# Kernel tuning notes

Hardware: AMD Instinct MI355X
Metric: run time of the kernel (lower is better)

Reference implementation:

```python
import jax, jax.numpy as jnp
import numpy as np

L, B, D = 2048, 8, 1024
EPS = 1e-5


def setup_inputs() -> dict:
    key = jax.random.key(0)
    k1, k2 = jax.random.split(key)
    x = jax.random.normal(k1, (L, B, D), dtype=jnp.float32)
    c = jnp.zeros((B, D), dtype=jnp.float32)
    # w_ufr: Linear(D, 3D); weight init normal(std=0.001), bias zero except
    # the reset-gate third which is filled with 2.0 (per the torch init).
    W = jax.random.normal(k2, (3 * D, D), dtype=jnp.float32) * 0.001
    b = jnp.zeros((3 * D,), dtype=jnp.float32).at[2 * D:].set(2.0)
    gamma = jnp.ones((D,), dtype=jnp.float32)
    beta = jnp.zeros((D,), dtype=jnp.float32)
    return {"x": x, "c": c, "W": W, "b": b, "gamma": gamma, "beta": beta}


def _layernorm(x, gamma, beta):
    mu = jnp.mean(x, axis=-1, keepdims=True)
    var = jnp.var(x, axis=-1, keepdims=True)
    return (x - mu) * jax.lax.rsqrt(var + EPS) * gamma + beta


def reference(x, c, W, b, gamma, beta):
    residual = x
    x_norm = _layernorm(x, gamma, beta)            # [L,B,D]
    ufr = jnp.einsum('lbd,ed->lbe', x_norm, W) + b  # [L,B,3D]
    u, f, r = jnp.split(ufr, 3, axis=-1)
    f_gate = jax.nn.sigmoid(f)
    r_gate = jax.nn.sigmoid(r)

    def step(c_prev, fu):
        f_t, u_t = fu
        c_t = f_t * c_prev + (1.0 - f_t) * u_t
        return c_t, c_t

    last_c, c_stack = jax.lax.scan(step, c, (f_gate, u))  # c_stack: [L,B,D]
    hs = r_gate * jnp.tanh(c_stack) + (1.0 - r_gate) * x_norm
    # dropout is identity in eval mode
    return residual + hs, last_c
```

## Files before the change

### kernel.cpp

```cpp
#include <hip/hip_runtime.h>
#include <hip/hip_bf16.h>

#define L_DIM 2048
#define B_DIM 8
#define D_DIM 1024
#define M_DIM (L_DIM * B_DIM)
#define N_DIM (3 * D_DIM)
#define K_DIM D_DIM
#define BD (B_DIM * D_DIM)
#define NCHUNK 64
#define CLEN (L_DIM / NCHUNK)

typedef __attribute__((ext_vector_type(8))) __bf16 bf16x8;
typedef __attribute__((ext_vector_type(4))) __bf16 bf16x4;
typedef __attribute__((ext_vector_type(4))) float f32x4;

#define GLOAD_LDS16(g, l)                                        \
  __builtin_amdgcn_global_load_lds(                              \
      (const __attribute__((address_space(1))) void*)(g),        \
      (__attribute__((address_space(3))) void*)(l), 16, 0, 0)

__device__ __forceinline__ float sigmoidf_(float v) {
  return 1.0f / (1.0f + __expf(-v));
}

__global__ __launch_bounds__(256) void ln_kernel(
    const float* __restrict__ x, const float* __restrict__ gamma,
    const float* __restrict__ beta, __bf16* __restrict__ xn) {
  const int row = blockIdx.x;
  const int tid = threadIdx.x;
  const float4 v = ((const float4*)(x + (size_t)row * D_DIM))[tid];
  float s  = v.x + v.y + v.z + v.w;
  float ss = v.x * v.x + v.y * v.y + v.z * v.z + v.w * v.w;
  #pragma unroll
  for (int off = 32; off > 0; off >>= 1) {
    s  += __shfl_xor(s, off);
    ss += __shfl_xor(ss, off);
  }
  __shared__ float sb[8];
  const int wid = tid >> 6, lane = tid & 63;
  if (lane == 0) { sb[wid] = s; sb[4 + wid] = ss; }
  __syncthreads();
  const float tot  = sb[0] + sb[1] + sb[2] + sb[3];
  const float tot2 = sb[4] + sb[5] + sb[6] + sb[7];
  const float mu  = tot * (1.0f / D_DIM);
  const float var = tot2 * (1.0f / D_DIM) - mu * mu;
  const float rstd = rsqrtf(var + 1e-5f);
  const float4 g  = ((const float4*)gamma)[tid];
  const float4 bt = ((const float4*)beta)[tid];
  bf16x4 o;
  o[0] = (__bf16)((v.x - mu) * rstd * g.x + bt.x);
  o[1] = (__bf16)((v.y - mu) * rstd * g.y + bt.y);
  o[2] = (__bf16)((v.z - mu) * rstd * g.z + bt.z);
  o[3] = (__bf16)((v.w - mu) * rstd * g.w + bt.w);
  ((bf16x4*)(xn + (size_t)row * D_DIM))[tid] = o;
}

__global__ __launch_bounds__(256) void wconv_kernel(
    const float* __restrict__ W, __bf16* __restrict__ Wb) {
  const size_t i = ((size_t)blockIdx.x * 256 + threadIdx.x) * 4;
  const float4 v = *(const float4*)(W + i);
  bf16x4 o;
  o[0] = (__bf16)v.x; o[1] = (__bf16)v.y; o[2] = (__bf16)v.z; o[3] = (__bf16)v.w;
  *(bf16x4*)(Wb + i) = o;
}

#define VMCNT(n) asm volatile("s_waitcnt vmcnt(" #n ")" ::: "memory")

__global__ __launch_bounds__(512, 4) void gemm256_kernel(
    const __bf16* __restrict__ A,
    const __bf16* __restrict__ Bm,
    const float* __restrict__ bias,
    __bf16* __restrict__ U, __bf16* __restrict__ FG, __bf16* __restrict__ RG) {
  __shared__ __bf16 lds[36864];
  const int tid = threadIdx.x;
  const int lane = tid & 63;
  const int wid = tid >> 6;
  const int wq = wid >> 1;
  const int wc = wid & 1;

  const int bid0 = blockIdx.x;
  const int bid = (bid0 & 7) * 192 + (bid0 >> 3);
  const int bm = bid / 24, bn = bid % 24;

#define BUFO(p) ((p) * 12288)

  const int srow  = tid >> 2;
  const int sslot = (tid & 3) ^ ((srow >> 1) & 3);
  auto stageA = [&](int kt2, int p) {
    const __bf16* gs = A + (size_t)(bm * 256 + srow) * K_DIM + kt2 * 32 +
                       sslot * 8;
    GLOAD_LDS16(gs, lds + BUFO(p) + tid * 8);
    GLOAD_LDS16(gs + (size_t)128 * K_DIM, lds + BUFO(p) + (tid + 512) * 8);
  };
  auto stageB = [&](int kt2, int p) {
    const __bf16* gs = Bm + (size_t)(bn * 128 + srow) * K_DIM + kt2 * 32 +
                       sslot * 8;
    GLOAD_LDS16(gs, lds + BUFO(p) + 8192 + tid * 8);
  };

  const int fr = lane & 15, fk = lane >> 4;
  const int swz = fk ^ ((fr >> 1) & 3);
  auto rdA = [&](int p, int m) {
    return *(const bf16x8*)(lds + BUFO(p) + (wq * 64 + m * 16 + fr) * 32 +
                            swz * 8);
  };
  auto rdB = [&](int p, int n) {
    return *(const bf16x8*)(lds + BUFO(p) + 8192 +
                            (wc * 64 + n * 16 + fr) * 32 + swz * 8);
  };

  f32x4 acc[4][4] = {};

  stageA(0, 0); stageB(0, 0);
  stageA(1, 1); stageB(1, 1);
  VMCNT(3);
  __builtin_amdgcn_s_barrier();

  int pc = 0;
  #pragma unroll 1
  for (int kt = 0; kt < 32; ++kt) {
    const int ps = pc >= 1 ? pc - 1 : 2;
    if (kt <= 29) { stageA(kt + 2, ps); stageB(kt + 2, ps); }

    bf16x8 a[4], b[4];
    #pragma unroll
    for (int m = 0; m < 4; ++m) a[m] = rdA(pc, m);
    #pragma unroll
    for (int n = 0; n < 4; ++n) b[n] = rdB(pc, n);

    __builtin_amdgcn_s_setprio(1);
    #pragma unroll
    for (int m = 0; m < 4; ++m)
      #pragma unroll
      for (int n = 0; n < 4; ++n)
        acc[m][n] = __builtin_amdgcn_mfma_f32_16x16x32_bf16(a[m], b[n],
                                                            acc[m][n], 0, 0, 0);
    __builtin_amdgcn_s_setprio(0);

    if (kt <= 29) { VMCNT(3); }
    else if (kt == 30) { VMCNT(0); }
    __builtin_amdgcn_s_barrier();
    pc = pc == 2 ? 0 : pc + 1;
  }

  const int seg = bn >> 3;
  __bf16* outb = (seg == 0) ? U : ((seg == 1) ? FG : RG);
  const int segcol0 = (bn & 7) * 128;

  float bv[4];
  #pragma unroll
  for (int n = 0; n < 4; ++n)
    bv[n] = bias[seg * 1024 + segcol0 + wc * 64 + n * 16 + fr];

  const int lrow = tid >> 4;
  const int chunk = tid & 15;
  #pragma unroll 1
  for (int h = 0; h < 2; ++h) {
    __syncthreads();
    if ((wq >> 1) == h) {
      const int lr0 = (wq & 1) * 64 + fk * 4;
      #pragma unroll
      for (int m = 0; m < 4; ++m)
        #pragma unroll
        for (int n = 0; n < 4; ++n)
          #pragma unroll
          for (int j = 0; j < 4; ++j) {
            float v = acc[m][n][j] + bv[n];
            if (seg != 0) v = sigmoidf_(v);
            lds[(lr0 + m * 16 + j) * 136 + wc * 64 + n * 16 + fr] = (__bf16)v;
          }
    }
    __syncthreads();
    #pragma unroll
    for (int it = 0; it < 4; ++it) {
      const int r = it * 32 + lrow;
      const bf16x8 val = *(const bf16x8*)(lds + r * 136 + chunk * 8);
      const size_t grow = (size_t)(bm * 256 + h * 128 + r);
      *(bf16x8*)(outb + grow * D_DIM + segcol0 + chunk * 8) = val;
    }
  }
}

__global__ __launch_bounds__(256) void scanA_kernel(
    const __bf16* __restrict__ fg, const __bf16* __restrict__ u,
    float* __restrict__ av) {
  const int ci = blockIdx.x;
  const int bd = blockIdx.y * 256 + threadIdx.x;
  float a = 1.0f, v = 0.0f;
  const size_t base = (size_t)ci * CLEN * BD + bd;
  #pragma unroll 8
  for (int i = 0; i < CLEN; ++i) {
    const size_t idx = base + (size_t)i * BD;
    const float f = (float)fg[idx];
    const float uu = (float)u[idx];
    a *= f;
    v = f * v + (1.0f - f) * uu;
  }
  av[(size_t)ci * BD + bd] = a;
  av[(size_t)NCHUNK * BD + (size_t)ci * BD + bd] = v;
}

__global__ __launch_bounds__(256) void scanB_kernel(
    const float* __restrict__ av, const float* __restrict__ c0,
    float* __restrict__ carries, float* __restrict__ out1) {
  const int bd = blockIdx.x * 256 + threadIdx.x;
  float c = c0[bd];
  #pragma unroll 8
  for (int ci = 0; ci < NCHUNK; ++ci) {
    carries[(size_t)ci * BD + bd] = c;
    c = av[(size_t)ci * BD + bd] * c + av[(size_t)NCHUNK * BD + (size_t)ci * BD + bd];
  }
  out1[bd] = c;
}

__global__ __launch_bounds__(256) void scanC_kernel(
    const __bf16* __restrict__ fg, const __bf16* __restrict__ u,
    const __bf16* __restrict__ rg, const __bf16* __restrict__ xn,
    const float* __restrict__ x, const float* __restrict__ carries,
    float* __restrict__ out0) {
  const int ci = blockIdx.x;
  const int bd = blockIdx.y * 256 + threadIdx.x;
  float c = carries[(size_t)ci * BD + bd];
  const size_t base = (size_t)ci * CLEN * BD + bd;
  #pragma unroll 4
  for (int i = 0; i < CLEN; ++i) {
    const size_t idx = base + (size_t)i * BD;
    const float f = (float)fg[idx];
    const float uu = (float)u[idx];
    c = f * c + (1.0f - f) * uu;
    const float r = (float)rg[idx];
    const float xnv = (float)xn[idx];
    const float hs = r * tanhf(c) + (1.0f - r) * xnv;
    out0[idx] = x[idx] + hs;
  }
}

extern "C" void kernel_launch(void* const* d_in, const int* in_sizes, int n_in,
                              void* d_out, int out_size, void* d_ws,
                              size_t ws_size, hipStream_t stream) {
  const float* x     = (const float*)d_in[0];
  const float* c0    = (const float*)d_in[1];
  const float* W     = (const float*)d_in[2];
  const float* bias  = (const float*)d_in[3];
  const float* gamma = (const float*)d_in[4];
  const float* beta  = (const float*)d_in[5];

  float* out0 = (float*)d_out;
  float* out1 = out0 + (size_t)M_DIM * D_DIM;

  char* ws = (char*)d_ws;
  __bf16* xn = (__bf16*)(ws + 0);
  __bf16* Wb = (__bf16*)(ws + 33554432);
  __bf16* U  = (__bf16*)(ws + 39845888);
  __bf16* FG = (__bf16*)(ws + 73400320);
  __bf16* RG = (__bf16*)(ws + 106954752);
  float* av      = (float*)(ws + 140509184);
  float* carries = (float*)(ws + 144703488);

  ln_kernel<<<M_DIM, 256, 0, stream>>>(x, gamma, beta, xn);
  wconv_kernel<<<(N_DIM * K_DIM / 4) / 256, 256, 0, stream>>>(W, Wb);
  gemm256_kernel<<<(M_DIM / 256) * (N_DIM / 128), 512, 0, stream>>>(
      xn, Wb, bias, U, FG, RG);
  scanA_kernel<<<dim3(NCHUNK, BD / 256), 256, 0, stream>>>(FG, U, av);
  scanB_kernel<<<BD / 256, 256, 0, stream>>>(av, c0, carries, out1);
  scanC_kernel<<<dim3(NCHUNK, BD / 256), 256, 0, stream>>>(
      FG, U, RG, xn, x, carries, out0);
}
```

Measured before the change: 228.2 us.

## Halve GEMM block threads and give each wave a 128x64 output tile

```diff
diff --git a/kernel.cpp b/kernel.cpp
--- a/kernel.cpp
+++ b/kernel.cpp
@@ -67,7 +67,7 @@
 
 #define VMCNT(n) asm volatile("s_waitcnt vmcnt(" #n ")" ::: "memory")
 
-__global__ __launch_bounds__(512, 4) void gemm256_kernel(
+__global__ __launch_bounds__(256, 2) void gemm256_kernel(
     const __bf16* __restrict__ A,
     const __bf16* __restrict__ Bm,
     const float* __restrict__ bias,
@@ -76,7 +76,7 @@
   const int tid = threadIdx.x;
   const int lane = tid & 63;
   const int wid = tid >> 6;
-  const int wq = wid >> 1;
+  const int wm = wid >> 1;
   const int wc = wid & 1;
 
   const int bid0 = blockIdx.x;
@@ -90,31 +90,36 @@
   auto stageA = [&](int kt2, int p) {
     const __bf16* gs = A + (size_t)(bm * 256 + srow) * K_DIM + kt2 * 32 +
                        sslot * 8;
-    GLOAD_LDS16(gs, lds + BUFO(p) + tid * 8);
-    GLOAD_LDS16(gs + (size_t)128 * K_DIM, lds + BUFO(p) + (tid + 512) * 8);
+    #pragma unroll
+    for (int i = 0; i < 4; ++i)
+      GLOAD_LDS16(gs + (size_t)(64 * i) * K_DIM,
+                  lds + BUFO(p) + (tid + 256 * i) * 8);
   };
   auto stageB = [&](int kt2, int p) {
     const __bf16* gs = Bm + (size_t)(bn * 128 + srow) * K_DIM + kt2 * 32 +
                        sslot * 8;
-    GLOAD_LDS16(gs, lds + BUFO(p) + 8192 + tid * 8);
+    #pragma unroll
+    for (int i = 0; i < 2; ++i)
+      GLOAD_LDS16(gs + (size_t)(64 * i) * K_DIM,
+                  lds + BUFO(p) + 8192 + (tid + 256 * i) * 8);
   };
 
   const int fr = lane & 15, fk = lane >> 4;
   const int swz = fk ^ ((fr >> 1) & 3);
   auto rdA = [&](int p, int m) {
-    return *(const bf16x8*)(lds + BUFO(p) + (wq * 64 + m * 16 + fr) * 32 +
-                            swz * 8);
+    return *(const bf16x8*)(lds + BUFO(p) +
+                            (wm * 128 + m * 16 + fr) * 32 + swz * 8);
   };
   auto rdB = [&](int p, int n) {
     return *(const bf16x8*)(lds + BUFO(p) + 8192 +
                             (wc * 64 + n * 16 + fr) * 32 + swz * 8);
   };
 
-  f32x4 acc[4][4] = {};
+  f32x4 acc[8][4] = {};
 
   stageA(0, 0); stageB(0, 0);
   stageA(1, 1); stageB(1, 1);
-  VMCNT(3);
+  VMCNT(6);
   __builtin_amdgcn_s_barrier();
 
   int pc = 0;
@@ -128,7 +133,6 @@
     for (int m = 0; m < 4; ++m) a[m] = rdA(pc, m);
     #pragma unroll
     for (int n = 0; n < 4; ++n) b[n] = rdB(pc, n);
-
     __builtin_amdgcn_s_setprio(1);
     #pragma unroll
     for (int m = 0; m < 4; ++m)
@@ -137,8 +141,18 @@
         acc[m][n] = __builtin_amdgcn_mfma_f32_16x16x32_bf16(a[m], b[n],
                                                             acc[m][n], 0, 0, 0);
     __builtin_amdgcn_s_setprio(0);
-
-    if (kt <= 29) { VMCNT(3); }
+    #pragma unroll
+    for (int m = 0; m < 4; ++m) a[m] = rdA(pc, m + 4);
+    __builtin_amdgcn_s_setprio(1);
+    #pragma unroll
+    for (int m = 0; m < 4; ++m)
+      #pragma unroll
+      for (int n = 0; n < 4; ++n)
+        acc[m + 4][n] = __builtin_amdgcn_mfma_f32_16x16x32_bf16(
+            a[m], b[n], acc[m + 4][n], 0, 0, 0);
+    __builtin_amdgcn_s_setprio(0);
+
+    if (kt <= 29) { VMCNT(6); }
     else if (kt == 30) { VMCNT(0); }
     __builtin_amdgcn_s_barrier();
     pc = pc == 2 ? 0 : pc + 1;
@@ -158,23 +172,23 @@
   #pragma unroll 1
   for (int h = 0; h < 2; ++h) {
     __syncthreads();
-    if ((wq >> 1) == h) {
-      const int lr0 = (wq & 1) * 64 + fk * 4;
+    if (wm == h) {
       #pragma unroll
-      for (int m = 0; m < 4; ++m)
+      for (int m = 0; m < 8; ++m)
         #pragma unroll
         for (int n = 0; n < 4; ++n)
           #pragma unroll
           for (int j = 0; j < 4; ++j) {
             float v = acc[m][n][j] + bv[n];
             if (seg != 0) v = sigmoidf_(v);
-            lds[(lr0 + m * 16 + j) * 136 + wc * 64 + n * 16 + fr] = (__bf16)v;
+            lds[(m * 16 + fk * 4 + j) * 136 + wc * 64 + n * 16 + fr] =
+                (__bf16)v;
           }
     }
     __syncthreads();
     #pragma unroll
-    for (int it = 0; it < 4; ++it) {
-      const int r = it * 32 + lrow;
+    for (int it = 0; it < 8; ++it) {
+      const int r = it * 16 + lrow;
       const bf16x8 val = *(const bf16x8*)(lds + r * 136 + chunk * 8);
       const size_t grow = (size_t)(bm * 256 + h * 128 + r);
       *(bf16x8*)(outb + grow * D_DIM + segcol0 + chunk * 8) = val;
@@ -260,7 +274,7 @@
 
   ln_kernel<<<M_DIM, 256, 0, stream>>>(x, gamma, beta, xn);
   wconv_kernel<<<(N_DIM * K_DIM / 4) / 256, 256, 0, stream>>>(W, Wb);
-  gemm256_kernel<<<(M_DIM / 256) * (N_DIM / 128), 512, 0, stream>>>(
+  gemm256_kernel<<<(M_DIM / 256) * (N_DIM / 128), 256, 0, stream>>>(
       xn, Wb, bias, U, FG, RG);
   scanA_kernel<<<dim3(NCHUNK, BD / 256), 256, 0, stream>>>(FG, U, av);
   scanB_kernel<<<BD / 256, 256, 0, stream>>>(av, c0, carries, out1);
```

New measurement: 227.8 us. Within noise of the previous version (-0.2%).

## Replace triple-buffered 256x128 GEMM with simple single-buffer 128x128 tile kernel

Applied to the files above, without the earlier changes.

```diff
diff --git a/kernel.cpp b/kernel.cpp
--- a/kernel.cpp
+++ b/kernel.cpp
@@ -65,83 +65,68 @@
   *(bf16x4*)(Wb + i) = o;
 }
 
-#define VMCNT(n) asm volatile("s_waitcnt vmcnt(" #n ")" ::: "memory")
-
-__global__ __launch_bounds__(512, 4) void gemm256_kernel(
+__global__ __launch_bounds__(256) void gemm_kernel(
     const __bf16* __restrict__ A,
     const __bf16* __restrict__ Bm,
     const float* __restrict__ bias,
     __bf16* __restrict__ U, __bf16* __restrict__ FG, __bf16* __restrict__ RG) {
-  __shared__ __bf16 lds[36864];
+  __shared__ __bf16 lds[17408];
   const int tid = threadIdx.x;
   const int lane = tid & 63;
   const int wid = tid >> 6;
-  const int wq = wid >> 1;
+  const int wm = wid >> 1;
   const int wc = wid & 1;
 
   const int bid0 = blockIdx.x;
-  const int bid = (bid0 & 7) * 192 + (bid0 >> 3);
+  const int bid = (bid0 & 7) * 384 + (bid0 >> 3);
   const int bm = bid / 24, bn = bid % 24;
 
-#define BUFO(p) ((p) * 12288)
-
-  const int srow  = tid >> 2;
-  const int sslot = (tid & 3) ^ ((srow >> 1) & 3);
-  auto stageA = [&](int kt2, int p) {
-    const __bf16* gs = A + (size_t)(bm * 256 + srow) * K_DIM + kt2 * 32 +
-                       sslot * 8;
-    GLOAD_LDS16(gs, lds + BUFO(p) + tid * 8);
-    GLOAD_LDS16(gs + (size_t)128 * K_DIM, lds + BUFO(p) + (tid + 512) * 8);
+  const int srow  = tid >> 3;
+  const int sslot = (tid & 7) ^ (srow & 7);
+  const __bf16* aSrc = A + (size_t)(bm * 128 + srow) * K_DIM + sslot * 8;
+  const __bf16* bSrc = Bm + (size_t)(bn * 128 + srow) * K_DIM + sslot * 8;
+
+  const int fr = lane & 15, fk = lane >> 4;
+  const int swzbase = fk ^ (fr & 7);
+  auto rdA = [&](int kk, int m) {
+    return *(const bf16x8*)(lds + (wm * 64 + m * 16 + fr) * 64 +
+                            ((kk * 4) ^ swzbase) * 8);
   };
-  auto stageB = [&](int kt2, int p) {
-    const __bf16* gs = Bm + (size_t)(bn * 128 + srow) * K_DIM + kt2 * 32 +
-                       sslot * 8;
-    GLOAD_LDS16(gs, lds + BUFO(p) + 8192 + tid * 8);
+  auto rdB = [&](int kk, int n) {
+    return *(const bf16x8*)(lds + 8192 + (wc * 64 + n * 16 + fr) * 64 +
+                            ((kk * 4) ^ swzbase) * 8);
   };
 
-  const int fr = lane & 15, fk = lane >> 4;
-  const int swz = fk ^ ((fr >> 1) & 3);
-  auto rdA = [&](int p, int m) {
-    return *(const bf16x8*)(lds + BUFO(p) + (wq * 64 + m * 16 + fr) * 32 +
-                            swz * 8);
-  };
-  auto rdB = [&](int p, int n) {
-    return *(const bf16x8*)(lds + BUFO(p) + 8192 +
-                            (wc * 64 + n * 16 + fr) * 32 + swz * 8);
-  };
-
   f32x4 acc[4][4] = {};
 
-  stageA(0, 0); stageB(0, 0);
-  stageA(1, 1); stageB(1, 1);
-  VMCNT(3);
-  __builtin_amdgcn_s_barrier();
-
-  int pc = 0;
   #pragma unroll 1
-  for (int kt = 0; kt < 32; ++kt) {
-    const int ps = pc >= 1 ? pc - 1 : 2;
-    if (kt <= 29) { stageA(kt + 2, ps); stageB(kt + 2, ps); }
-
-    bf16x8 a[4], b[4];
+  for (int kt = 0; kt < 16; ++kt) {
+    __syncthreads();
     #pragma unroll
-    for (int m = 0; m < 4; ++m) a[m] = rdA(pc, m);
+    for (int i = 0; i < 4; ++i) {
+      GLOAD_LDS16(aSrc + (size_t)(32 * i) * K_DIM + kt * 64,
+                  lds + (tid + 256 * i) * 8);
+      GLOAD_LDS16(bSrc + (size_t)(32 * i) * K_DIM + kt * 64,
+                  lds + 8192 + (tid + 256 * i) * 8);
+    }
+    __syncthreads();
+
     #pragma unroll
-    for (int n = 0; n < 4; ++n) b[n] = rdB(pc, n);
-
-    __builtin_amdgcn_s_setprio(1);
-    #pragma unroll
-    for (int m = 0; m < 4; ++m)
-      #pragma unroll
-      for (int n = 0; n < 4; ++n)
-        acc[m][n] = __builtin_amdgcn_mfma_f32_16x16x32_bf16(a[m], b[n],
-                                                            acc[m][n], 0, 0, 0);
-    __builtin_amdgcn_s_setprio(0);
-
-    if (kt <= 29) { VMCNT(3); }
-    else if (kt == 30) { VMCNT(0); }
-    __builtin_amdgcn_s_barrier();
-    pc = pc == 2 ? 0 : pc + 1;
+    for (int kk = 0; kk < 2; ++kk) {
+      bf16x8 a[4], b[4];
+      #pragma unroll
+      for (int m = 0; m < 4; ++m) a[m] = rdA(kk, m);
+      #pragma unroll
+      for (int n = 0; n < 4; ++n) b[n] = rdB(kk, n);
+      __builtin_amdgcn_s_setprio(1);
+      #pragma unroll
+      for (int m = 0; m < 4; ++m)
+        #pragma unroll
+        for (int n = 0; n < 4; ++n)
+          acc[m][n] = __builtin_amdgcn_mfma_f32_16x16x32_bf16(
+              a[m], b[n], acc[m][n], 0, 0, 0);
+      __builtin_amdgcn_s_setprio(0);
+    }
   }
 
   const int seg = bn >> 3;
@@ -153,32 +138,27 @@
   for (int n = 0; n < 4; ++n)
     bv[n] = bias[seg * 1024 + segcol0 + wc * 64 + n * 16 + fr];
 
+  __syncthreads();
+  #pragma unroll
+  for (int m = 0; m < 4; ++m)
+    #pragma unroll
+    for (int n = 0; n < 4; ++n)
+      #pragma unroll
+      for (int j = 0; j < 4; ++j) {
+        float v = acc[m][n][j] + bv[n];
+        if (seg != 0) v = sigmoidf_(v);
+        lds[(wm * 64 + m * 16 + fk * 4 + j) * 136 + wc * 64 + n * 16 + fr] =
+            (__bf16)v;
+      }
+  __syncthreads();
   const int lrow = tid >> 4;
   const int chunk = tid & 15;
-  #pragma unroll 1
-  for (int h = 0; h < 2; ++h) {
-    __syncthreads();
-    if ((wq >> 1) == h) {
-      const int lr0 = (wq & 1) * 64 + fk * 4;
-      #pragma unroll
-      for (int m = 0; m < 4; ++m)
-        #pragma unroll
-        for (int n = 0; n < 4; ++n)
-          #pragma unroll
-          for (int j = 0; j < 4; ++j) {
-            float v = acc[m][n][j] + bv[n];
-            if (seg != 0) v = sigmoidf_(v);
-            lds[(lr0 + m * 16 + j) * 136 + wc * 64 + n * 16 + fr] = (__bf16)v;
-          }
-    }
-    __syncthreads();
-    #pragma unroll
-    for (int it = 0; it < 4; ++it) {
-      const int r = it * 32 + lrow;
-      const bf16x8 val = *(const bf16x8*)(lds + r * 136 + chunk * 8);
-      const size_t grow = (size_t)(bm * 256 + h * 128 + r);
-      *(bf16x8*)(outb + grow * D_DIM + segcol0 + chunk * 8) = val;
-    }
+  #pragma unroll
+  for (int it = 0; it < 8; ++it) {
+    const int r = it * 16 + lrow;
+    const bf16x8 val = *(const bf16x8*)(lds + r * 136 + chunk * 8);
+    const size_t grow = (size_t)(bm * 128 + r);
+    *(bf16x8*)(outb + grow * D_DIM + segcol0 + chunk * 8) = val;
   }
 }
 
@@ -260,7 +240,7 @@
 
   ln_kernel<<<M_DIM, 256, 0, stream>>>(x, gamma, beta, xn);
   wconv_kernel<<<(N_DIM * K_DIM / 4) / 256, 256, 0, stream>>>(W, Wb);
-  gemm256_kernel<<<(M_DIM / 256) * (N_DIM / 128), 512, 0, stream>>>(
+  gemm_kernel<<<(M_DIM / 128) * (N_DIM / 128), 256, 0, stream>>>(
       xn, Wb, bias, U, FG, RG);
   scanA_kernel<<<dim3(NCHUNK, BD / 256), 256, 0, stream>>>(FG, U, av);
   scanB_kernel<<<BD / 256, 256, 0, stream>>>(av, c0, carries, out1);
```

Measured after the change: 216.0 us. 5.4% less time.
